# Kernel optimization log

Hardware: AMD Instinct MI355X
Metric: run time of the kernel (lower is better)

Reference implementation:

```python
import jax, jax.numpy as jnp
import numpy as np

B, C, H, W = 8, 128, 64, 64  # dim = in_channels = 128, N = H*W = 4096
TEMP = float(C) ** 0.5


def _proj(x, w, b):
    # 1x1 conv: [B,C,H,W] x [D,C] -> [B,D,H,W]
    return jnp.einsum('bchw,dc->bdhw', x, w) + b[None, :, None, None]


def setup_inputs() -> dict:
    key = jax.random.key(0)
    ks = jax.random.split(key, 6)
    std = 0.01
    x = jax.random.normal(ks[0], (B, C, H, W), dtype=jnp.float32)
    wq = jax.random.normal(ks[1], (C, C), dtype=jnp.float32) * std
    wk = jax.random.normal(ks[2], (C, C), dtype=jnp.float32) * std
    wv = jax.random.normal(ks[3], (C, C), dtype=jnp.float32) * std
    wo = jax.random.normal(ks[4], (C, C), dtype=jnp.float32) * std
    zeros = jnp.zeros((C,), dtype=jnp.float32)
    return {"x": x, "wq": wq, "bq": zeros, "wk": wk, "bk": zeros,
            "wv": wv, "bv": zeros, "wo": wo, "bo": zeros}


def reference(x, wq, bq, wk, bk, wv, bv, wo, bo):
    n, c, h, w = x.shape
    N = h * w
    q = _proj(x, wq, bq).reshape(n, c, N)          # [B, D, N]
    k = _proj(x, wk, bk).reshape(n, c, N)          # [B, D, N]
    v = _proj(x, wv, bv).reshape(n, c, N)          # [B, D, N]
    # attn[b, i, j] = sum_d q[b,d,i] * k[b,d,j] / temp
    attn = jnp.einsum('bdi,bdj->bij', q, k) / TEMP  # [B, N, N]
    attn = jax.nn.softmax(attn, axis=-1)
    # y[b, d, i] = sum_j attn[b,i,j] * v[b,d,j]
    y = jnp.einsum('bij,bdj->bdi', attn, v).reshape(n, c, h, w)
    y = _proj(y, wo, bo)                            # conv_out
    return x + y                                    # identity residual
```

## Files before the change

kernel.cpp:

```cpp
#include <hip/hip_runtime.h>


typedef float  f32x4  __attribute__((ext_vector_type(4)));
typedef float  f32x16 __attribute__((ext_vector_type(16)));
typedef short  s16x8  __attribute__((ext_vector_type(8)));
typedef short  s16x4  __attribute__((ext_vector_type(4)));
typedef unsigned uint4v __attribute__((ext_vector_type(4)));

#define MFMA16(A, Bb, Cc) __builtin_amdgcn_mfma_f32_16x16x32_bf16(A, Bb, Cc, 0, 0, 0)
#define MFMA32(A, Bb, Cc) __builtin_amdgcn_mfma_f32_32x32x16_bf16(A, Bb, Cc, 0, 0, 0)

#define BATCH 8
#define DIM   128
#define NN    4096
#define NSPLIT 2
#define JCHUNK (NN / NSPLIT)
#define NT    (JCHUNK / 64)
#define Q_SCALE 0.12751649736784776f

#if __has_builtin(__builtin_amdgcn_exp2f)
#define EXP2(x) __builtin_amdgcn_exp2f(x)
#else
#define EXP2(x) exp2f(x)
#endif

__device__ __forceinline__ unsigned short f2bf(float f) {
  union { float f; unsigned u; } v; v.f = f;
  unsigned r = v.u + 0x7FFFu + ((v.u >> 16) & 1u);
  return (unsigned short)(r >> 16);
}
__device__ __forceinline__ float bf2f(unsigned short h) {
  union { unsigned u; float f; } v; v.u = ((unsigned)h) << 16;
  return v.f;
}
__device__ __forceinline__ s16x8 cvt8(const float* src) {
  float4 a = *(const float4*)src;
  float4 b = *(const float4*)(src + 4);
  s16x8 f;
  f[0] = (short)f2bf(a.x); f[1] = (short)f2bf(a.y);
  f[2] = (short)f2bf(a.z); f[3] = (short)f2bf(a.w);
  f[4] = (short)f2bf(b.x); f[5] = (short)f2bf(b.y);
  f[6] = (short)f2bf(b.z); f[7] = (short)f2bf(b.w);
  return f;
}

__global__ __launch_bounds__(256) void qkv_kernel(
    const float* __restrict__ x,
    const float* __restrict__ wq, const float* __restrict__ wk,
    const float* __restrict__ wv,
    const float* __restrict__ bq, const float* __restrict__ bk,
    const float* __restrict__ bv,
    unsigned short* __restrict__ qt,
    unsigned short* __restrict__ kt,
    unsigned short* __restrict__ vv) {
  __shared__ float xs[DIM * 68];
  __shared__ unsigned short wls[DIM * 136];
  const int b = blockIdx.y;
  const int i0 = blockIdx.x * 64;
  const int tid = threadIdx.x;

  for (int idx = tid; idx < 2048; idx += 256) {
    int c = idx >> 4, i4 = idx & 15;
    float4 val = *(const float4*)(x + ((size_t)(b * DIM + c)) * NN + i0 + i4 * 4);
    xs[c * 68 + i4 * 4 + 0] = val.x;
    xs[c * 68 + i4 * 4 + 1] = val.y;
    xs[c * 68 + i4 * 4 + 2] = val.z;
    xs[c * 68 + i4 * 4 + 3] = val.w;
  }
  __syncthreads();

  const int w = tid >> 6, lane = tid & 63, quad = lane >> 4, l15 = lane & 15;
  const int iloc = w * 16 + l15;

  s16x8 bfrag[4];
#pragma unroll
  for (int ch = 0; ch < 4; ch++) {
    s16x8 f;
#pragma unroll
    for (int jj = 0; jj < 8; jj++) {
      int c = ch * 32 + quad * 8 + jj;
      f[jj] = (short)f2bf(xs[c * 68 + iloc]);
    }
    bfrag[ch] = f;
  }

  const int i = i0 + iloc;
  const int wr = tid >> 4, wc = tid & 15;

  for (int z = 0; z < 3; z++) {
    __syncthreads();
    const float* wsrc = (z == 0) ? wq : (z == 1) ? wk : wv;
#pragma unroll
    for (int it = 0; it < 8; it++) {
      const int row = it * 16 + wr;
      *(s16x8*)(&wls[row * 136 + wc * 8]) = cvt8(wsrc + row * DIM + wc * 8);
    }
    __syncthreads();

    const float* bias = (z == 0) ? bq : (z == 1) ? bk : bv;
    const float sc = (z == 0) ? Q_SCALE : 1.0f;

    for (int t = 0; t < 8; t++) {
      const int dl = t * 16;
      f32x4 acc = {0.f, 0.f, 0.f, 0.f};
#pragma unroll
      for (int ch = 0; ch < 4; ch++) {
        s16x8 af = *(const s16x8*)(&wls[(dl + l15) * 136 + ch * 32 + quad * 8]);
        acc = MFMA16(af, bfrag[ch], acc);
      }
      if (z < 2) {
        unsigned short* dstb = (z == 0) ? qt : kt;
        s16x4 o;
#pragma unroll
        for (int r = 0; r < 4; r++) {
          int d = dl + quad * 4 + r;
          o[r] = (short)f2bf((acc[r] + bias[d]) * sc);
        }
        *(s16x4*)(dstb + ((size_t)b * NN + i) * DIM + dl + quad * 4) = o;
      } else {
#pragma unroll
        for (int r = 0; r < 4; r++) {
          int d = dl + quad * 4 + r;
          vv[((size_t)b * DIM + d) * NN + i] = f2bf(acc[r] + bias[d]);
        }
      }
    }
  }
}

__global__ __launch_bounds__(256, 2) void attn_kernel(
    const unsigned short* __restrict__ qt,
    const unsigned short* __restrict__ kt,
    const unsigned short* __restrict__ vv,
    unsigned short* __restrict__ o_part,
    float* __restrict__ l_part) {
  __shared__ unsigned short sh[32768];
  const int b = blockIdx.y;
  const int i0 = blockIdx.x * 128;
  const int split = blockIdx.z;
  const int jbase = split * JCHUNK;
  const int tid = threadIdx.x;
  const int w = tid >> 6, lane = tid & 63;
  const int l31 = lane & 31, h = lane >> 5;

  const unsigned short* kb = kt + (size_t)b * NN * DIM;
  const unsigned short* vb = vv + (size_t)b * DIM * NN;

  s16x8 qfrag[8];
  {
    const unsigned short* qrow =
        qt + ((size_t)b * NN + i0 + w * 32 + l31) * DIM + h * 8;
#pragma unroll
    for (int kc = 0; kc < 8; kc++)
      qfrag[kc] = *(const s16x8*)(qrow + kc * 16);
  }

  f32x16 acc[4];
#pragma unroll
  for (int mt = 0; mt < 4; mt++)
#pragma unroll
    for (int e = 0; e < 16; e++) acc[mt][e] = 0.f;
  float l_acc = 0.f;

  const int kr = tid >> 4, kc_ = tid & 15;
  const int vr = tid >> 3, vc = tid & 7;
  const int vch0 = (vc & 1) ? (vc - 1) : vc;
  const int vch1 = (vc & 1) ? vc : (vc + 1);
  const int vpos = (vc & 1) * 4;

  s16x8 kpre[4], vpre[4];

#pragma unroll
  for (int it = 0; it < 4; it++) {
    kpre[it] = *(const s16x8*)(kb + (size_t)(jbase + it * 16 + kr) * DIM + kc_ * 8);
    vpre[it] = *(const s16x8*)(vb + (size_t)(it * 32 + vr) * NN + jbase + vc * 8);
  }
#pragma unroll
  for (int it = 0; it < 4; it++) {
    const int r = it * 16 + kr;
    *(s16x8*)(sh + (((r << 4) + (kc_ ^ (r & 15))) << 3)) = kpre[it];
    const int r2 = it * 32 + vr;
    union { s16x8 v8; s16x4 v4[2]; } sp; sp.v8 = vpre[it];
    *(s16x4*)(sh + 8192 + (((r2 << 3) + (vch0 ^ (r2 & 7))) << 3) + vpos) = sp.v4[0];
    *(s16x4*)(sh + 8192 + (((r2 << 3) + (vch1 ^ (r2 & 7))) << 3) + vpos) = sp.v4[1];
  }
#pragma unroll
  for (int it = 0; it < 4; it++) {
    kpre[it] = *(const s16x8*)(kb + (size_t)(jbase + 64 + it * 16 + kr) * DIM + kc_ * 8);
    vpre[it] = *(const s16x8*)(vb + (size_t)(it * 32 + vr) * NN + jbase + 64 + vc * 8);
  }

  for (int t = 0; t < NT; t++) {
    __syncthreads();

    if (t + 1 < NT) {
      unsigned short* wb = sh + ((~t & 1) << 14);
#pragma unroll
      for (int it = 0; it < 4; it++) {
        const int r = it * 16 + kr;
        *(s16x8*)(wb + (((r << 4) + (kc_ ^ (r & 15))) << 3)) = kpre[it];
        const int r2 = it * 32 + vr;
        union { s16x8 v8; s16x4 v4[2]; } sp; sp.v8 = vpre[it];
        *(s16x4*)(wb + 8192 + (((r2 << 3) + (vch0 ^ (r2 & 7))) << 3) + vpos) = sp.v4[0];
        *(s16x4*)(wb + 8192 + (((r2 << 3) + (vch1 ^ (r2 & 7))) << 3) + vpos) = sp.v4[1];
      }
    }

    if (t + 2 < NT) {
      const int jn = jbase + (t + 2) * 64;
#pragma unroll
      for (int it = 0; it < 4; it++) {
        kpre[it] = *(const s16x8*)(kb + (size_t)(jn + it * 16 + kr) * DIM + kc_ * 8);
        vpre[it] = *(const s16x8*)(vb + (size_t)(it * 32 + vr) * NN + jn + vc * 8);
      }
    }

    const unsigned short* rK = sh + ((t & 1) << 14);
    const unsigned short* rV = rK + 8192;

#pragma unroll
    for (int jt = 0; jt < 2; jt++) {
      f32x16 S;
#pragma unroll
      for (int e = 0; e < 16; e++) S[e] = 0.f;
      const int j = jt * 32 + l31;
      __builtin_amdgcn_s_setprio(1);
#pragma unroll
      for (int kc = 0; kc < 8; kc++) {
        s16x8 kf = *(const s16x8*)(rK + (((j << 4) + ((2 * kc + h) ^ (j & 15))) << 3));
        S = MFMA32(kf, qfrag[kc], S);
      }
      __builtin_amdgcn_s_setprio(0);
      unsigned pk[8];
#pragma unroll
      for (int p = 0; p < 8; p++) {
        float e0 = EXP2(S[2 * p]), e1 = EXP2(S[2 * p + 1]);
        l_acc += e0 + e1;
        union { float f; unsigned u; } u0, u1; u0.f = e0; u1.f = e1;
        pk[p] = __builtin_amdgcn_perm(u1.u, u0.u, 0x07060302u);
      }
      __builtin_amdgcn_s_setprio(1);
#pragma unroll
      for (int bl = 0; bl < 2; bl++) {
        union { uint4v u; s16x8 v; } pu;
        pu.u[0] = pk[4 * bl + 0]; pu.u[1] = pk[4 * bl + 1];
        pu.u[2] = pk[4 * bl + 2]; pu.u[3] = pk[4 * bl + 3];
        const s16x8 pf = pu.v;
        const int c0 = (jt * 2 + bl) * 2 + h;
#pragma unroll
        for (int mt = 0; mt < 4; mt++) {
          const int d = mt * 32 + l31;
          s16x8 vf = *(const s16x8*)(rV + (((d << 3) + (c0 ^ (d & 7))) << 3));
          acc[mt] = MFMA32(vf, pf, acc[mt]);
        }
      }
      __builtin_amdgcn_s_setprio(0);
    }
  }

  const float l_tot = l_acc + __shfl_xor(l_acc, 32, 64);

  __syncthreads();
  unsigned short* ep = sh + w * 4096;
#pragma unroll
  for (int mt = 0; mt < 4; mt++)
#pragma unroll
    for (int reg = 0; reg < 16; reg++) {
      int d = mt * 32 + (reg & 3) + 8 * (reg >> 2) + 4 * h;
      int dc = d >> 3;
      ep[(l31 << 7) + ((dc ^ (l31 & 15)) << 3) + (d & 7)] = f2bf(acc[mt][reg]);
    }
  __syncthreads();
#pragma unroll
  for (int it = 0; it < 8; it++) {
    int qr = it * 4 + (lane >> 4), cr = lane & 15;
    s16x8 v = *(const s16x8*)(ep + (qr << 7) + ((cr ^ (qr & 15)) << 3));
    *(s16x8*)(o_part + (((size_t)split * BATCH + b) * NN + i0 + w * 32 + qr) * DIM +
              cr * 8) = v;
  }
  if (lane < 32)
    l_part[((size_t)split * BATCH + b) * NN + i0 + w * 32 + lane] = l_tot;
}

__global__ __launch_bounds__(256) void outp_kernel(
    const float* __restrict__ x,
    const float* __restrict__ wo,
    const float* __restrict__ bo,
    const unsigned short* __restrict__ o_part,
    const float* __restrict__ l_part,
    float* __restrict__ out) {
  __shared__ unsigned short ytile[64 * 136];
  __shared__ unsigned short wls[DIM * 136];
  __shared__ float invl[64];
  const int b = blockIdx.y;
  const int i0 = blockIdx.x * 64;
  const int tid = threadIdx.x;
  const int wr = tid >> 4, wc = tid & 15;

#pragma unroll
  for (int it = 0; it < 8; it++) {
    const int row = it * 16 + wr;
    *(s16x8*)(&wls[row * 136 + wc * 8]) = cvt8(wo + row * DIM + wc * 8);
  }

  if (tid < 64) {
    float l = 0.f;
#pragma unroll
    for (int s = 0; s < NSPLIT; s++)
      l += l_part[((size_t)s * BATCH + b) * NN + i0 + tid];
    invl[tid] = 1.0f / l;
  }
  __syncthreads();

#pragma unroll
  for (int k = 0; k < 4; k++) {
    int slot = k * 256 + tid;
    int i = slot >> 4, g = slot & 15;
    float o[8] = {0.f, 0.f, 0.f, 0.f, 0.f, 0.f, 0.f, 0.f};
#pragma unroll
    for (int s = 0; s < NSPLIT; s++) {
      s16x8 ov = *(const s16x8*)(o_part +
                                 (((size_t)s * BATCH + b) * NN + i0 + i) * DIM + g * 8);
#pragma unroll
      for (int jj = 0; jj < 8; jj++) o[jj] += bf2f((unsigned short)ov[jj]);
    }
    const float inv = invl[i];
    s16x8 f;
#pragma unroll
    for (int jj = 0; jj < 8; jj++) f[jj] = (short)f2bf(o[jj] * inv);
    *(s16x8*)(&ytile[i * 136 + g * 8]) = f;
  }
  __syncthreads();

  const int w = tid >> 6, lane = tid & 63, quad = lane >> 4, l15 = lane & 15;
  const int i = i0 + w * 16 + l15;

  s16x8 bfrag[4];
#pragma unroll
  for (int ch = 0; ch < 4; ch++)
    bfrag[ch] = *(const s16x8*)(&ytile[(w * 16 + l15) * 136 + ch * 32 + quad * 8]);

  for (int t = 0; t < 8; t++) {
    f32x4 acc = {0.f, 0.f, 0.f, 0.f};
#pragma unroll
    for (int ch = 0; ch < 4; ch++) {
      s16x8 af = *(const s16x8*)(&wls[(t * 16 + l15) * 136 + ch * 32 + quad * 8]);
      acc = MFMA16(af, bfrag[ch], acc);
    }
#pragma unroll
    for (int r = 0; r < 4; r++) {
      int d = t * 16 + quad * 4 + r;
      size_t idx = ((size_t)b * DIM + d) * NN + i;
      out[idx] = x[idx] + acc[r] + bo[d];
    }
  }
}

extern "C" void kernel_launch(void* const* d_in, const int* in_sizes, int n_in,
                              void* d_out, int out_size, void* d_ws, size_t ws_size,
                              hipStream_t stream) {
  const float* x  = (const float*)d_in[0];
  const float* wq = (const float*)d_in[1];
  const float* bq = (const float*)d_in[2];
  const float* wk = (const float*)d_in[3];
  const float* bk = (const float*)d_in[4];
  const float* wv = (const float*)d_in[5];
  const float* bv = (const float*)d_in[6];
  const float* wo = (const float*)d_in[7];
  const float* bo = (const float*)d_in[8];
  float* out = (float*)d_out;

  unsigned short* ws  = (unsigned short*)d_ws;
  unsigned short* qt  = ws;
  unsigned short* kt  = qt + (size_t)BATCH * NN * DIM;
  unsigned short* vv  = kt + (size_t)BATCH * NN * DIM;
  unsigned short* o_part = vv + (size_t)BATCH * NN * DIM;
  float* l_part = (float*)(o_part + (size_t)NSPLIT * BATCH * NN * DIM);

  hipLaunchKernelGGL(qkv_kernel, dim3(64, 8), dim3(256), 0, stream,
                     x, wq, wk, wv, bq, bk, bv, qt, kt, vv);
  hipLaunchKernelGGL(attn_kernel, dim3(32, 8, NSPLIT), dim3(256), 0, stream,
                     qt, kt, vv, o_part, l_part);
  hipLaunchKernelGGL(outp_kernel, dim3(64, 8), dim3(256), 0, stream,
                     x, wo, bo, o_part, l_part, out);
}
```

Measured before the change: 174.0 us.

## Fuse split-combine and output projection into attention kernel via atomic counter

The output projection kernel is removed. Its work now runs as an epilogue inside the attention kernel. Each attention block bumps a per-tile atomic counter after writing its partial result, and the last of the two splits to finish combines the partials, normalizes, applies the 1x1 output projection and adds the residual. The counters are zeroed in the QKV kernel. This drops one kernel launch and its tail. In exchange, shared memory grows, the final epilogue runs serialized on half the blocks, and correctness depends on threadfence ordering of the partial writes.

```diff
diff --git a/kernel.cpp b/kernel.cpp
--- a/kernel.cpp
+++ b/kernel.cpp
@@ -52,12 +52,15 @@
     const float* __restrict__ bv,
     unsigned short* __restrict__ qt,
     unsigned short* __restrict__ kt,
-    unsigned short* __restrict__ vv) {
+    unsigned short* __restrict__ vv,
+    int* __restrict__ cnt) {
   __shared__ float xs[DIM * 68];
   __shared__ unsigned short wls[DIM * 136];
   const int b = blockIdx.y;
   const int i0 = blockIdx.x * 64;
   const int tid = threadIdx.x;
+
+  if (blockIdx.x == 0 && blockIdx.y == 0 && tid < 256) cnt[tid] = 0;
 
   for (int idx = tid; idx < 2048; idx += 256) {
     int c = idx >> 4, i4 = idx & 15;
@@ -132,9 +135,15 @@
     const unsigned short* __restrict__ qt,
     const unsigned short* __restrict__ kt,
     const unsigned short* __restrict__ vv,
+    const float* __restrict__ x,
+    const float* __restrict__ wo,
+    const float* __restrict__ bo,
     unsigned short* __restrict__ o_part,
-    float* __restrict__ l_part) {
-  __shared__ unsigned short sh[32768];
+    float* __restrict__ l_part,
+    int* __restrict__ cnt,
+    float* __restrict__ out) {
+  __shared__ unsigned short sh[35072];
+  __shared__ int s_old;
   const int b = blockIdx.y;
   const int i0 = blockIdx.x * 128;
   const int split = blockIdx.z;
@@ -280,30 +289,24 @@
   }
   if (lane < 32)
     l_part[((size_t)split * BATCH + b) * NN + i0 + w * 32 + lane] = l_tot;
-}
-
-__global__ __launch_bounds__(256) void outp_kernel(
-    const float* __restrict__ x,
-    const float* __restrict__ wo,
-    const float* __restrict__ bo,
-    const unsigned short* __restrict__ o_part,
-    const float* __restrict__ l_part,
-    float* __restrict__ out) {
-  __shared__ unsigned short ytile[64 * 136];
-  __shared__ unsigned short wls[DIM * 136];
-  __shared__ float invl[64];
-  const int b = blockIdx.y;
-  const int i0 = blockIdx.x * 64;
-  const int tid = threadIdx.x;
+
+  __threadfence();
+  if (tid == 0) s_old = atomicAdd(&cnt[blockIdx.y * 32 + blockIdx.x], 1);
+  __syncthreads();
+  if (s_old == 0) return;
+  __threadfence();
+
+  unsigned short* wls   = sh;
+  unsigned short* ytile = sh + DIM * 136;
+  float* invl = (float*)(sh + 2 * DIM * 136);
+
   const int wr = tid >> 4, wc = tid & 15;
-
 #pragma unroll
   for (int it = 0; it < 8; it++) {
     const int row = it * 16 + wr;
     *(s16x8*)(&wls[row * 136 + wc * 8]) = cvt8(wo + row * DIM + wc * 8);
   }
-
-  if (tid < 64) {
+  if (tid < 128) {
     float l = 0.f;
 #pragma unroll
     for (int s = 0; s < NSPLIT; s++)
@@ -313,7 +316,7 @@
   __syncthreads();
 
 #pragma unroll
-  for (int k = 0; k < 4; k++) {
+  for (int k = 0; k < 8; k++) {
     int slot = k * 256 + tid;
     int i = slot >> 4, g = slot & 15;
     float o[8] = {0.f, 0.f, 0.f, 0.f, 0.f, 0.f, 0.f, 0.f};
@@ -332,26 +335,27 @@
   }
   __syncthreads();
 
-  const int w = tid >> 6, lane = tid & 63, quad = lane >> 4, l15 = lane & 15;
-  const int i = i0 + w * 16 + l15;
-
-  s16x8 bfrag[4];
-#pragma unroll
-  for (int ch = 0; ch < 4; ch++)
-    bfrag[ch] = *(const s16x8*)(&ytile[(w * 16 + l15) * 136 + ch * 32 + quad * 8]);
-
-  for (int t = 0; t < 8; t++) {
-    f32x4 acc = {0.f, 0.f, 0.f, 0.f};
-#pragma unroll
-    for (int ch = 0; ch < 4; ch++) {
-      s16x8 af = *(const s16x8*)(&wls[(t * 16 + l15) * 136 + ch * 32 + quad * 8]);
-      acc = MFMA16(af, bfrag[ch], acc);
-    }
-#pragma unroll
-    for (int r = 0; r < 4; r++) {
-      int d = t * 16 + quad * 4 + r;
-      size_t idx = ((size_t)b * DIM + d) * NN + i;
-      out[idx] = x[idx] + acc[r] + bo[d];
+  const int quad = lane >> 4, l15 = lane & 15;
+#pragma unroll
+  for (int half = 0; half < 2; half++) {
+    const int il = half * 64 + w * 16 + l15;
+    s16x8 bfr[4];
+#pragma unroll
+    for (int ch = 0; ch < 4; ch++)
+      bfr[ch] = *(const s16x8*)(&ytile[il * 136 + ch * 32 + quad * 8]);
+    for (int t = 0; t < 8; t++) {
+      f32x4 a4 = {0.f, 0.f, 0.f, 0.f};
+#pragma unroll
+      for (int ch = 0; ch < 4; ch++) {
+        s16x8 af = *(const s16x8*)(&wls[(t * 16 + l15) * 136 + ch * 32 + quad * 8]);
+        a4 = MFMA16(af, bfr[ch], a4);
+      }
+#pragma unroll
+      for (int r = 0; r < 4; r++) {
+        int d = t * 16 + quad * 4 + r;
+        size_t idx = ((size_t)b * DIM + d) * NN + i0 + il;
+        out[idx] = x[idx] + a4[r] + bo[d];
+      }
     }
   }
 }
@@ -376,11 +380,10 @@
   unsigned short* vv  = kt + (size_t)BATCH * NN * DIM;
   unsigned short* o_part = vv + (size_t)BATCH * NN * DIM;
   float* l_part = (float*)(o_part + (size_t)NSPLIT * BATCH * NN * DIM);
+  int* cnt = (int*)(l_part + (size_t)NSPLIT * BATCH * NN);
 
   hipLaunchKernelGGL(qkv_kernel, dim3(64, 8), dim3(256), 0, stream,
-                     x, wq, wk, wv, bq, bk, bv, qt, kt, vv);
+                     x, wq, wk, wv, bq, bk, bv, qt, kt, vv, cnt);
   hipLaunchKernelGGL(attn_kernel, dim3(32, 8, NSPLIT), dim3(256), 0, stream,
-                     qt, kt, vv, o_part, l_part);
-  hipLaunchKernelGGL(outp_kernel, dim3(64, 8), dim3(256), 0, stream,
-                     x, wo, bo, o_part, l_part, out);
-}
+                     qt, kt, vv, x, wo, bo, o_part, l_part, cnt, out);
+}
```

Result: slower. 237.4 us (+36.4%).

## Split QKV projection across grid z and prefetch o_part loads in output kernel

Applied to the files above, without the earlier changes.

The QKV projection kernel now launches one block per (tile, batch, projection) with grid z=3, so each block handles a single weight matrix instead of looping over all three. The x tile is stored in shared memory as bf16, and each weight load overlaps with the x load. The output kernel issues all partial-output global loads up front, before the weight conversion, to hide their latency. Launch bounds hint three blocks per CU. The trade-off is that x is read and converted three times, once per projection block.

```diff
diff --git a/kernel.cpp b/kernel.cpp
--- a/kernel.cpp
+++ b/kernel.cpp
@@ -44,7 +44,7 @@
   return f;
 }
 
-__global__ __launch_bounds__(256) void qkv_kernel(
+__global__ __launch_bounds__(256, 3) void qkv_kernel(
     const float* __restrict__ x,
     const float* __restrict__ wq, const float* __restrict__ wk,
     const float* __restrict__ wv,
@@ -53,24 +53,33 @@
     unsigned short* __restrict__ qt,
     unsigned short* __restrict__ kt,
     unsigned short* __restrict__ vv) {
-  __shared__ float xs[DIM * 68];
+  __shared__ unsigned short xs16[DIM * 72];
   __shared__ unsigned short wls[DIM * 136];
   const int b = blockIdx.y;
   const int i0 = blockIdx.x * 64;
+  const int z = blockIdx.z;
   const int tid = threadIdx.x;
 
-  for (int idx = tid; idx < 2048; idx += 256) {
-    int c = idx >> 4, i4 = idx & 15;
-    float4 val = *(const float4*)(x + ((size_t)(b * DIM + c)) * NN + i0 + i4 * 4);
-    xs[c * 68 + i4 * 4 + 0] = val.x;
-    xs[c * 68 + i4 * 4 + 1] = val.y;
-    xs[c * 68 + i4 * 4 + 2] = val.z;
-    xs[c * 68 + i4 * 4 + 3] = val.w;
+  const float* wsrc = (z == 0) ? wq : (z == 1) ? wk : wv;
+  const float* bias = (z == 0) ? bq : (z == 1) ? bk : bv;
+  const float sc = (z == 0) ? Q_SCALE : 1.0f;
+
+  const int wr = tid >> 4, wc = tid & 15;
+#pragma unroll
+  for (int it = 0; it < 8; it++) {
+    const int row = it * 16 + wr;
+    *(s16x8*)(&wls[row * 136 + wc * 8]) = cvt8(wsrc + row * DIM + wc * 8);
+  }
+  for (int idx = tid; idx < 1024; idx += 256) {
+    int c = idx >> 3, i8 = idx & 7;
+    *(s16x8*)(&xs16[c * 72 + i8 * 8]) =
+        cvt8(x + ((size_t)(b * DIM + c)) * NN + i0 + i8 * 8);
   }
   __syncthreads();
 
   const int w = tid >> 6, lane = tid & 63, quad = lane >> 4, l15 = lane & 15;
   const int iloc = w * 16 + l15;
+  const int i = i0 + iloc;
 
   s16x8 bfrag[4];
 #pragma unroll
@@ -79,50 +88,33 @@
 #pragma unroll
     for (int jj = 0; jj < 8; jj++) {
       int c = ch * 32 + quad * 8 + jj;
-      f[jj] = (short)f2bf(xs[c * 68 + iloc]);
+      f[jj] = (short)xs16[c * 72 + iloc];
     }
     bfrag[ch] = f;
   }
 
-  const int i = i0 + iloc;
-  const int wr = tid >> 4, wc = tid & 15;
-
-  for (int z = 0; z < 3; z++) {
-    __syncthreads();
-    const float* wsrc = (z == 0) ? wq : (z == 1) ? wk : wv;
-#pragma unroll
-    for (int it = 0; it < 8; it++) {
-      const int row = it * 16 + wr;
-      *(s16x8*)(&wls[row * 136 + wc * 8]) = cvt8(wsrc + row * DIM + wc * 8);
-    }
-    __syncthreads();
-
-    const float* bias = (z == 0) ? bq : (z == 1) ? bk : bv;
-    const float sc = (z == 0) ? Q_SCALE : 1.0f;
-
-    for (int t = 0; t < 8; t++) {
-      const int dl = t * 16;
-      f32x4 acc = {0.f, 0.f, 0.f, 0.f};
-#pragma unroll
-      for (int ch = 0; ch < 4; ch++) {
-        s16x8 af = *(const s16x8*)(&wls[(dl + l15) * 136 + ch * 32 + quad * 8]);
-        acc = MFMA16(af, bfrag[ch], acc);
-      }
-      if (z < 2) {
-        unsigned short* dstb = (z == 0) ? qt : kt;
-        s16x4 o;
-#pragma unroll
-        for (int r = 0; r < 4; r++) {
-          int d = dl + quad * 4 + r;
-          o[r] = (short)f2bf((acc[r] + bias[d]) * sc);
-        }
-        *(s16x4*)(dstb + ((size_t)b * NN + i) * DIM + dl + quad * 4) = o;
-      } else {
-#pragma unroll
-        for (int r = 0; r < 4; r++) {
-          int d = dl + quad * 4 + r;
-          vv[((size_t)b * DIM + d) * NN + i] = f2bf(acc[r] + bias[d]);
-        }
+  for (int t = 0; t < 8; t++) {
+    const int dl = t * 16;
+    f32x4 acc = {0.f, 0.f, 0.f, 0.f};
+#pragma unroll
+    for (int ch = 0; ch < 4; ch++) {
+      s16x8 af = *(const s16x8*)(&wls[(dl + l15) * 136 + ch * 32 + quad * 8]);
+      acc = MFMA16(af, bfrag[ch], acc);
+    }
+    if (z < 2) {
+      unsigned short* dstb = (z == 0) ? qt : kt;
+      s16x4 o;
+#pragma unroll
+      for (int r = 0; r < 4; r++) {
+        int d = dl + quad * 4 + r;
+        o[r] = (short)f2bf((acc[r] + bias[d]) * sc);
+      }
+      *(s16x4*)(dstb + ((size_t)b * NN + i) * DIM + dl + quad * 4) = o;
+    } else {
+#pragma unroll
+      for (int r = 0; r < 4; r++) {
+        int d = dl + quad * 4 + r;
+        vv[((size_t)b * DIM + d) * NN + i] = f2bf(acc[r] + bias[d]);
       }
     }
   }
@@ -194,15 +186,15 @@
     __syncthreads();
 
     if (t + 1 < NT) {
-      unsigned short* wb = sh + ((~t & 1) << 14);
+      unsigned short* wb2 = sh + ((~t & 1) << 14);
 #pragma unroll
       for (int it = 0; it < 4; it++) {
         const int r = it * 16 + kr;
-        *(s16x8*)(wb + (((r << 4) + (kc_ ^ (r & 15))) << 3)) = kpre[it];
+        *(s16x8*)(wb2 + (((r << 4) + (kc_ ^ (r & 15))) << 3)) = kpre[it];
         const int r2 = it * 32 + vr;
         union { s16x8 v8; s16x4 v4[2]; } sp; sp.v8 = vpre[it];
-        *(s16x4*)(wb + 8192 + (((r2 << 3) + (vch0 ^ (r2 & 7))) << 3) + vpos) = sp.v4[0];
-        *(s16x4*)(wb + 8192 + (((r2 << 3) + (vch1 ^ (r2 & 7))) << 3) + vpos) = sp.v4[1];
+        *(s16x4*)(wb2 + 8192 + (((r2 << 3) + (vch0 ^ (r2 & 7))) << 3) + vpos) = sp.v4[0];
+        *(s16x4*)(wb2 + 8192 + (((r2 << 3) + (vch1 ^ (r2 & 7))) << 3) + vpos) = sp.v4[1];
       }
     }
 
@@ -282,7 +274,7 @@
     l_part[((size_t)split * BATCH + b) * NN + i0 + w * 32 + lane] = l_tot;
 }
 
-__global__ __launch_bounds__(256) void outp_kernel(
+__global__ __launch_bounds__(256, 3) void outp_kernel(
     const float* __restrict__ x,
     const float* __restrict__ wo,
     const float* __restrict__ bo,
@@ -295,8 +287,17 @@
   const int b = blockIdx.y;
   const int i0 = blockIdx.x * 64;
   const int tid = threadIdx.x;
+  const int ir = tid >> 4, g = tid & 15;
+
+  s16x8 ov[4][2];
+#pragma unroll
+  for (int k = 0; k < 4; k++)
+#pragma unroll
+    for (int s = 0; s < NSPLIT; s++)
+      ov[k][s] = *(const s16x8*)(o_part +
+          (((size_t)s * BATCH + b) * NN + i0 + k * 16 + ir) * DIM + g * 8);
+
   const int wr = tid >> 4, wc = tid & 15;
-
 #pragma unroll
   for (int it = 0; it < 8; it++) {
     const int row = it * 16 + wr;
@@ -314,20 +315,14 @@
 
 #pragma unroll
   for (int k = 0; k < 4; k++) {
-    int slot = k * 256 + tid;
-    int i = slot >> 4, g = slot & 15;
-    float o[8] = {0.f, 0.f, 0.f, 0.f, 0.f, 0.f, 0.f, 0.f};
-#pragma unroll
-    for (int s = 0; s < NSPLIT; s++) {
-      s16x8 ov = *(const s16x8*)(o_part +
-                                 (((size_t)s * BATCH + b) * NN + i0 + i) * DIM + g * 8);
-#pragma unroll
-      for (int jj = 0; jj < 8; jj++) o[jj] += bf2f((unsigned short)ov[jj]);
-    }
+    const int i = k * 16 + ir;
     const float inv = invl[i];
     s16x8 f;
 #pragma unroll
-    for (int jj = 0; jj < 8; jj++) f[jj] = (short)f2bf(o[jj] * inv);
+    for (int jj = 0; jj < 8; jj++) {
+      float o = bf2f((unsigned short)ov[k][0][jj]) + bf2f((unsigned short)ov[k][1][jj]);
+      f[jj] = (short)f2bf(o * inv);
+    }
     *(s16x8*)(&ytile[i * 136 + g * 8]) = f;
   }
   __syncthreads();
@@ -377,7 +372,7 @@
   unsigned short* o_part = vv + (size_t)BATCH * NN * DIM;
   float* l_part = (float*)(o_part + (size_t)NSPLIT * BATCH * NN * DIM);
 
-  hipLaunchKernelGGL(qkv_kernel, dim3(64, 8), dim3(256), 0, stream,
+  hipLaunchKernelGGL(qkv_kernel, dim3(64, 8, 3), dim3(256), 0, stream,
                      x, wq, wk, wv, bq, bk, bv, qt, kt, vv);
   hipLaunchKernelGGL(attn_kernel, dim3(32, 8, NSPLIT), dim3(256), 0, stream,
                      qt, kt, vv, o_part, l_part);
```

Result: slower. 178.9 us (+2.8%).
